# Performance work log

Hardware: AMD Instinct MI355X
Metric: run time of the kernel (lower is better)

Reference implementation:

```python
import jax, jax.numpy as jnp
import numpy as np

EPS = 1e-8

def setup_inputs() -> dict:
    key = jax.random.key(0)
    k1, k2, k3, k4, k5 = jax.random.split(key, 5)
    B, N, M, D = 64, 65536, 64, 256
    return {
        "embeddings": jax.random.normal(k1, (B, D), dtype=jnp.float32),
        "w_prev": jax.random.uniform(k2, (B, N), dtype=jnp.float32),
        "memory": jax.random.normal(k3, (B, N, M), dtype=jnp.float32),
        "W": jax.random.normal(k4, (D, M + 6), dtype=jnp.float32) * 0.05,
        "b": jax.random.normal(k5, (M + 6,), dtype=jnp.float32) * 0.01,
    }


def reference(embeddings, w_prev, memory, W, b):
    Mdim = memory.shape[-1]
    a = embeddings @ W + b  # [B, M+6]
    k = a[:, :Mdim]                                   # key
    beta = jax.nn.softplus(a[:, Mdim:Mdim + 1])       # key strength
    g = jax.nn.sigmoid(a[:, Mdim + 1:Mdim + 2])       # interpolation gate
    s = jax.nn.softmax(a[:, Mdim + 2:Mdim + 5], axis=1)  # 3-wide shift
    gamma = 1.0 + jax.nn.softplus(a[:, Mdim + 5:Mdim + 6])  # sharpening

    # content addressing: cosine similarity then softmax
    kn = k / (jnp.linalg.norm(k, axis=1, keepdims=True) + EPS)          # [B, M]
    mn = memory / (jnp.linalg.norm(memory, axis=2, keepdims=True) + EPS)  # [B, N, M]
    sim = jnp.einsum('bm,bnm->bn', kn, mn)                              # [B, N]
    wc = jax.nn.softmax(beta * sim, axis=1)

    # gated interpolation with previous weights
    wg = g * wc + (1.0 - g) * w_prev

    # circular shift convolution (shifts -1, 0, +1)
    wt = (s[:, 0:1] * jnp.roll(wg, 1, axis=1)
          + s[:, 1:2] * wg
          + s[:, 2:3] * jnp.roll(wg, -1, axis=1))

    # sharpening
    wp = wt ** gamma
    w = wp / (jnp.sum(wp, axis=1, keepdims=True) + EPS)

    # weighted memory read
    read = jnp.einsum('bn,bnm->bm', w, memory)
    return read, w
```

## Files before the change

### kernel.cpp

```cpp
#include <hip/hip_runtime.h>
#include <math.h>

#define EPS 1e-8f

constexpr int B = 64;
constexpr int N = 65536;
constexpr int M = 64;
constexpr int D = 256;
constexpr int A = M + 6;

constexpr size_t OFF_KN   = 0;
constexpr size_t OFF_SCAL = OFF_KN + (size_t)B * M;
constexpr size_t OFF_E    = OFF_SCAL + (size_t)B * 8;
constexpr size_t OFF_ZP   = OFF_E + (size_t)B * N;
constexpr size_t OFF_SP   = OFF_ZP + (size_t)B * 64;
constexpr size_t OFF_RP   = OFF_SP + (size_t)B * 16;

__device__ __forceinline__ float softplusf(float x) {
    return (x > 20.0f) ? x : log1pf(expf(x));
}

__global__ void k1_controller(const float* __restrict__ emb,
                              const float* __restrict__ Wm,
                              const float* __restrict__ bias,
                              float* __restrict__ kn,
                              float* __restrict__ scal) {
    int b = blockIdx.x;
    int t = threadIdx.x;
    __shared__ float se[D];
    __shared__ float sa[A];
    __shared__ float snorm;
    se[t] = emb[(size_t)b * D + t];
    __syncthreads();
    if (t < A) {
        float acc = bias[t];
        for (int d = 0; d < D; ++d) acc += se[d] * Wm[(size_t)d * A + t];
        sa[t] = acc;
    }
    __syncthreads();
    if (t == 0) {
        float s = 0.f;
        for (int j = 0; j < M; ++j) s += sa[j] * sa[j];
        snorm = sqrtf(s) + EPS;
        float beta = softplusf(sa[M]);
        float g = 1.f / (1.f + expf(-sa[M + 1]));
        float s0 = sa[M + 2], s1 = sa[M + 3], s2 = sa[M + 4];
        float mx = fmaxf(s0, fmaxf(s1, s2));
        float e0 = expf(s0 - mx), e1 = expf(s1 - mx), e2 = expf(s2 - mx);
        float Zs = e0 + e1 + e2;
        float gamma = 1.f + softplusf(sa[M + 5]);
        scal[b * 8 + 0] = beta;
        scal[b * 8 + 1] = g;
        scal[b * 8 + 2] = e0 / Zs;
        scal[b * 8 + 3] = e1 / Zs;
        scal[b * 8 + 4] = e2 / Zs;
        scal[b * 8 + 5] = gamma;
    }
    __syncthreads();
    if (t < M) kn[b * M + t] = sa[t] / snorm;
}

__global__ void k2_sim(const float* __restrict__ mem,
                       const float* __restrict__ kn,
                       const float* __restrict__ scal,
                       float* __restrict__ e,
                       float* __restrict__ zpart) {
    const int ROWS = 1024;
    int b = blockIdx.y;
    int base = blockIdx.x * ROWS;
    int t = threadIdx.x;
    int gid = t >> 4, q = t & 15;
    float beta = scal[b * 8 + 0];
    const float4 knq = reinterpret_cast<const float4*>(kn + (size_t)b * M)[q];
    const float4* mrow = reinterpret_cast<const float4*>(mem + (size_t)b * N * M);
    float* eb = e + (size_t)b * N;
    float lsum = 0.f;
    #pragma unroll 4
    for (int r = gid; r < ROWS; r += 16) {
        int n = base + r;
        float4 v = mrow[(size_t)n * 16 + q];
        float dot = v.x * knq.x + v.y * knq.y + v.z * knq.z + v.w * knq.w;
        float nrm = v.x * v.x + v.y * v.y + v.z * v.z + v.w * v.w;
        #pragma unroll
        for (int msk = 8; msk >= 1; msk >>= 1) {
            dot += __shfl_xor(dot, msk);
            nrm += __shfl_xor(nrm, msk);
        }
        float ev = expf(beta * (dot / (sqrtf(nrm) + EPS)));
        if (q == 0) { eb[n] = ev; lsum += ev; }
    }
    __shared__ float red[16];
    if (q == 0) red[gid] = lsum;
    __syncthreads();
    if (t == 0) {
        float s = 0.f;
        #pragma unroll
        for (int i = 0; i < 16; ++i) s += red[i];
        zpart[b * 64 + blockIdx.x] = s;
    }
}

__global__ void k4_wp(const float* __restrict__ e,
                      const float* __restrict__ wprev,
                      const float* __restrict__ scal,
                      const float* __restrict__ zpart,
                      float* __restrict__ wout,
                      float* __restrict__ spart) {
    int b = blockIdx.y;
    int bx = blockIdx.x;
    int t = threadIdx.x;
    float Z = 0.f;
    const float* zp = zpart + b * 64;
    #pragma unroll
    for (int i = 0; i < 64; ++i) Z += zp[i];
    float g   = scal[b * 8 + 1];
    float s0  = scal[b * 8 + 2];
    float s1  = scal[b * 8 + 3];
    float s2  = scal[b * 8 + 4];
    float gam = scal[b * 8 + 5];
    float c1 = g / Z;
    float c2 = 1.f - g;
    const float* eb = e + (size_t)b * N;
    const float* wb = wprev + (size_t)b * N;
    float* wo = wout + (size_t)b * N;
    float lsum = 0.f;
    #pragma unroll
    for (int i = 0; i < 4; ++i) {
        int n0 = bx * 4096 + (i * 256 + t) * 4;
        float4 e4 = *reinterpret_cast<const float4*>(eb + n0);
        float4 w4 = *reinterpret_cast<const float4*>(wb + n0);
        int nm = (n0 - 1) & (N - 1);
        int np = (n0 + 4) & (N - 1);
        float em = eb[nm], ep = eb[np];
        float wm = wb[nm], wp5 = wb[np];
        float wgm = c1 * em   + c2 * wm;
        float wg0 = c1 * e4.x + c2 * w4.x;
        float wg1 = c1 * e4.y + c2 * w4.y;
        float wg2 = c1 * e4.z + c2 * w4.z;
        float wg3 = c1 * e4.w + c2 * w4.w;
        float wg4 = c1 * ep   + c2 * wp5;
        float p0 = powf(s0 * wgm + s1 * wg0 + s2 * wg1, gam);
        float p1 = powf(s0 * wg0 + s1 * wg1 + s2 * wg2, gam);
        float p2 = powf(s0 * wg1 + s1 * wg2 + s2 * wg3, gam);
        float p3 = powf(s0 * wg2 + s1 * wg3 + s2 * wg4, gam);
        lsum += (p0 + p1) + (p2 + p3);
        *reinterpret_cast<float4*>(wo + n0) = make_float4(p0, p1, p2, p3);
    }
    __shared__ float red[256];
    red[t] = lsum;
    __syncthreads();
    for (int k = 128; k >= 1; k >>= 1) {
        if (t < k) red[t] += red[t + k];
        __syncthreads();
    }
    if (t == 0) spart[b * 16 + bx] = red[0];
}

__global__ void k5_read(const float* __restrict__ mem,
                        float* __restrict__ wout,
                        const float* __restrict__ spart,
                        float* __restrict__ readpart) {
    const int ROWS = 1024;
    int b = blockIdx.y;
    int base = blockIdx.x * ROWS;
    int t = threadIdx.x;
    int gid = t >> 4, q = t & 15;
    float S = 0.f;
    const float* sp = spart + b * 16;
    #pragma unroll
    for (int i = 0; i < 16; ++i) S += sp[i];
    float invS = 1.f / (S + EPS);
    const float4* mrow = reinterpret_cast<const float4*>(mem + (size_t)b * N * M);
    float* wb = wout + (size_t)b * N;
    float4 acc = make_float4(0.f, 0.f, 0.f, 0.f);
    #pragma unroll 4
    for (int r = gid; r < ROWS; r += 16) {
        int n = base + r;
        float wv = wb[n] * invS;
        float4 v = mrow[(size_t)n * 16 + q];
        acc.x += wv * v.x;
        acc.y += wv * v.y;
        acc.z += wv * v.z;
        acc.w += wv * v.w;
    }
    __shared__ float sacc[16][64];
    sacc[gid][q * 4 + 0] = acc.x;
    sacc[gid][q * 4 + 1] = acc.y;
    sacc[gid][q * 4 + 2] = acc.z;
    sacc[gid][q * 4 + 3] = acc.w;
    __syncthreads();
    #pragma unroll
    for (int i = 0; i < 4; ++i) {
        int n = base + i * 256 + t;
        wb[n] = wb[n] * invS;
    }
    if (t < 64) {
        float s = 0.f;
        #pragma unroll
        for (int g2 = 0; g2 < 16; ++g2) s += sacc[g2][t];
        readpart[((size_t)b * 64 + blockIdx.x) * 64 + t] = s;
    }
}

__global__ void k6_read_reduce(const float* __restrict__ readpart,
                               float* __restrict__ readout) {
    int b = blockIdx.x;
    int m = threadIdx.x;
    float s = 0.f;
    #pragma unroll
    for (int kb = 0; kb < 64; ++kb) s += readpart[((size_t)b * 64 + kb) * 64 + m];
    readout[b * 64 + m] = s;
}

extern "C" void kernel_launch(void* const* d_in, const int* in_sizes, int n_in,
                              void* d_out, int out_size, void* d_ws, size_t ws_size,
                              hipStream_t stream) {
    const float* emb   = (const float*)d_in[0];
    const float* wprev = (const float*)d_in[1];
    const float* mem   = (const float*)d_in[2];
    const float* Wm    = (const float*)d_in[3];
    const float* bias  = (const float*)d_in[4];

    float* out = (float*)d_out;
    float* readout = out;
    float* wout    = out + (size_t)B * M;

    float* ws = (float*)d_ws;
    float* kn   = ws + OFF_KN;
    float* scal = ws + OFF_SCAL;
    float* e    = ws + OFF_E;
    float* zp   = ws + OFF_ZP;
    float* sp   = ws + OFF_SP;
    float* rp   = ws + OFF_RP;

    k1_controller<<<dim3(B), dim3(256), 0, stream>>>(emb, Wm, bias, kn, scal);
    k2_sim<<<dim3(N / 1024, B), dim3(256), 0, stream>>>(mem, kn, scal, e, zp);
    k4_wp<<<dim3(N / 4096, B), dim3(256), 0, stream>>>(e, wprev, scal, zp, wout, sp);
    k5_read<<<dim3(N / 1024, B), dim3(256), 0, stream>>>(mem, wout, sp, rp);
    k6_read_reduce<<<dim3(B), dim3(64), 0, stream>>>(rp, readout);
}
```

Baseline: 457.7 us.

## Chunk batches and fuse shift/sharpen with read so memory rereads hit cache

Processes the batch in chunks of 8 so the similarity pass and the fused weighting+read pass touch a memory slice small enough to stay in the last-level cache. Fuses the interpolation, shift and sharpening into the read kernel, deferring normalization to a separate w-normalize kernel and scaling the reduced read by 1/S. Intent is to avoid a second full DRAM pass over the large memory tensor. Risks lower occupancy per chunk launch and redundant per-row scalar work in 16 lanes.

```diff
diff --git a/kernel.cpp b/kernel.cpp
--- a/kernel.cpp
+++ b/kernel.cpp
@@ -8,13 +8,14 @@
 constexpr int M = 64;
 constexpr int D = 256;
 constexpr int A = M + 6;
+constexpr int CHUNK = 8;
 
 constexpr size_t OFF_KN   = 0;
 constexpr size_t OFF_SCAL = OFF_KN + (size_t)B * M;
 constexpr size_t OFF_E    = OFF_SCAL + (size_t)B * 8;
 constexpr size_t OFF_ZP   = OFF_E + (size_t)B * N;
 constexpr size_t OFF_SP   = OFF_ZP + (size_t)B * 64;
-constexpr size_t OFF_RP   = OFF_SP + (size_t)B * 16;
+constexpr size_t OFF_RP   = OFF_SP + (size_t)B * 64;
 
 __device__ __forceinline__ float softplusf(float x) {
     return (x > 20.0f) ? x : log1pf(expf(x));
@@ -64,9 +65,10 @@
                        const float* __restrict__ kn,
                        const float* __restrict__ scal,
                        float* __restrict__ e,
-                       float* __restrict__ zpart) {
+                       float* __restrict__ zpart,
+                       int b0) {
     const int ROWS = 1024;
-    int b = blockIdx.y;
+    int b = b0 + blockIdx.y;
     int base = blockIdx.x * ROWS;
     int t = threadIdx.x;
     int gid = t >> 4, q = t & 15;
@@ -75,7 +77,7 @@
     const float4* mrow = reinterpret_cast<const float4*>(mem + (size_t)b * N * M);
     float* eb = e + (size_t)b * N;
     float lsum = 0.f;
-    #pragma unroll 4
+    #pragma unroll 8
     for (int r = gid; r < ROWS; r += 16) {
         int n = base + r;
         float4 v = mrow[(size_t)n * 16 + q];
@@ -100,15 +102,21 @@
     }
 }
 
-__global__ void k4_wp(const float* __restrict__ e,
-                      const float* __restrict__ wprev,
-                      const float* __restrict__ scal,
-                      const float* __restrict__ zpart,
-                      float* __restrict__ wout,
-                      float* __restrict__ spart) {
-    int b = blockIdx.y;
+__global__ void k45_fused(const float* __restrict__ mem,
+                          const float* __restrict__ e,
+                          const float* __restrict__ wprev,
+                          const float* __restrict__ scal,
+                          const float* __restrict__ zpart,
+                          float* __restrict__ wout,
+                          float* __restrict__ spart,
+                          float* __restrict__ readpart,
+                          int b0) {
+    const int ROWS = 1024;
+    int b = b0 + blockIdx.y;
     int bx = blockIdx.x;
+    int base = bx * ROWS;
     int t = threadIdx.x;
+    int gid = t >> 4, q = t & 15;
     float Z = 0.f;
     const float* zp = zpart + b * 64;
     #pragma unroll
@@ -120,96 +128,80 @@
     float gam = scal[b * 8 + 5];
     float c1 = g / Z;
     float c2 = 1.f - g;
+    const float4* mrow = reinterpret_cast<const float4*>(mem + (size_t)b * N * M);
     const float* eb = e + (size_t)b * N;
     const float* wb = wprev + (size_t)b * N;
     float* wo = wout + (size_t)b * N;
+    float4 acc = make_float4(0.f, 0.f, 0.f, 0.f);
     float lsum = 0.f;
-    #pragma unroll
-    for (int i = 0; i < 4; ++i) {
-        int n0 = bx * 4096 + (i * 256 + t) * 4;
-        float4 e4 = *reinterpret_cast<const float4*>(eb + n0);
-        float4 w4 = *reinterpret_cast<const float4*>(wb + n0);
-        int nm = (n0 - 1) & (N - 1);
-        int np = (n0 + 4) & (N - 1);
-        float em = eb[nm], ep = eb[np];
-        float wm = wb[nm], wp5 = wb[np];
-        float wgm = c1 * em   + c2 * wm;
-        float wg0 = c1 * e4.x + c2 * w4.x;
-        float wg1 = c1 * e4.y + c2 * w4.y;
-        float wg2 = c1 * e4.z + c2 * w4.z;
-        float wg3 = c1 * e4.w + c2 * w4.w;
-        float wg4 = c1 * ep   + c2 * wp5;
-        float p0 = powf(s0 * wgm + s1 * wg0 + s2 * wg1, gam);
-        float p1 = powf(s0 * wg0 + s1 * wg1 + s2 * wg2, gam);
-        float p2 = powf(s0 * wg1 + s1 * wg2 + s2 * wg3, gam);
-        float p3 = powf(s0 * wg2 + s1 * wg3 + s2 * wg4, gam);
-        lsum += (p0 + p1) + (p2 + p3);
-        *reinterpret_cast<float4*>(wo + n0) = make_float4(p0, p1, p2, p3);
-    }
-    __shared__ float red[256];
-    red[t] = lsum;
-    __syncthreads();
-    for (int k = 128; k >= 1; k >>= 1) {
-        if (t < k) red[t] += red[t + k];
-        __syncthreads();
-    }
-    if (t == 0) spart[b * 16 + bx] = red[0];
-}
-
-__global__ void k5_read(const float* __restrict__ mem,
-                        float* __restrict__ wout,
-                        const float* __restrict__ spart,
-                        float* __restrict__ readpart) {
-    const int ROWS = 1024;
-    int b = blockIdx.y;
-    int base = blockIdx.x * ROWS;
-    int t = threadIdx.x;
-    int gid = t >> 4, q = t & 15;
-    float S = 0.f;
-    const float* sp = spart + b * 16;
-    #pragma unroll
-    for (int i = 0; i < 16; ++i) S += sp[i];
-    float invS = 1.f / (S + EPS);
-    const float4* mrow = reinterpret_cast<const float4*>(mem + (size_t)b * N * M);
-    float* wb = wout + (size_t)b * N;
-    float4 acc = make_float4(0.f, 0.f, 0.f, 0.f);
     #pragma unroll 4
     for (int r = gid; r < ROWS; r += 16) {
         int n = base + r;
-        float wv = wb[n] * invS;
+        int nm = (n - 1) & (N - 1);
+        int np = (n + 1) & (N - 1);
+        float wgm = c1 * eb[nm] + c2 * wb[nm];
+        float wg0 = c1 * eb[n]  + c2 * wb[n];
+        float wgp = c1 * eb[np] + c2 * wb[np];
+        float wt = s0 * wgm + s1 * wg0 + s2 * wgp;
+        float wp = powf(wt, gam);
         float4 v = mrow[(size_t)n * 16 + q];
-        acc.x += wv * v.x;
-        acc.y += wv * v.y;
-        acc.z += wv * v.z;
-        acc.w += wv * v.w;
+        acc.x += wp * v.x;
+        acc.y += wp * v.y;
+        acc.z += wp * v.z;
+        acc.w += wp * v.w;
+        if (q == 0) { wo[n] = wp; lsum += wp; }
     }
     __shared__ float sacc[16][64];
+    __shared__ float sred[16];
     sacc[gid][q * 4 + 0] = acc.x;
     sacc[gid][q * 4 + 1] = acc.y;
     sacc[gid][q * 4 + 2] = acc.z;
     sacc[gid][q * 4 + 3] = acc.w;
-    __syncthreads();
-    #pragma unroll
-    for (int i = 0; i < 4; ++i) {
-        int n = base + i * 256 + t;
-        wb[n] = wb[n] * invS;
-    }
+    if (q == 0) sred[gid] = lsum;
+    __syncthreads();
     if (t < 64) {
         float s = 0.f;
         #pragma unroll
         for (int g2 = 0; g2 < 16; ++g2) s += sacc[g2][t];
-        readpart[((size_t)b * 64 + blockIdx.x) * 64 + t] = s;
-    }
+        readpart[((size_t)b * 64 + bx) * 64 + t] = s;
+    }
+    if (t == 0) {
+        float s = 0.f;
+        #pragma unroll
+        for (int i = 0; i < 16; ++i) s += sred[i];
+        spart[b * 64 + bx] = s;
+    }
+}
+
+__global__ void k7_wnorm(float* __restrict__ wout,
+                         const float* __restrict__ spart) {
+    int b = blockIdx.y;
+    float S = 0.f;
+    const float* sp = spart + b * 64;
+    #pragma unroll
+    for (int i = 0; i < 64; ++i) S += sp[i];
+    float invS = 1.f / (S + EPS);
+    size_t idx = (size_t)b * (N / 4) + blockIdx.x * 256 + threadIdx.x;
+    float4* w4 = reinterpret_cast<float4*>(wout);
+    float4 v = w4[idx];
+    v.x *= invS; v.y *= invS; v.z *= invS; v.w *= invS;
+    w4[idx] = v;
 }
 
 __global__ void k6_read_reduce(const float* __restrict__ readpart,
+                               const float* __restrict__ spart,
                                float* __restrict__ readout) {
     int b = blockIdx.x;
     int m = threadIdx.x;
+    float S = 0.f;
+    const float* sp = spart + b * 64;
+    #pragma unroll
+    for (int i = 0; i < 64; ++i) S += sp[i];
+    float invS = 1.f / (S + EPS);
     float s = 0.f;
     #pragma unroll
     for (int kb = 0; kb < 64; ++kb) s += readpart[((size_t)b * 64 + kb) * 64 + m];
-    readout[b * 64 + m] = s;
+    readout[b * 64 + m] = s * invS;
 }
 
 extern "C" void kernel_launch(void* const* d_in, const int* in_sizes, int n_in,
@@ -234,8 +226,12 @@
     float* rp   = ws + OFF_RP;
 
     k1_controller<<<dim3(B), dim3(256), 0, stream>>>(emb, Wm, bias, kn, scal);
-    k2_sim<<<dim3(N / 1024, B), dim3(256), 0, stream>>>(mem, kn, scal, e, zp);
-    k4_wp<<<dim3(N / 4096, B), dim3(256), 0, stream>>>(e, wprev, scal, zp, wout, sp);
-    k5_read<<<dim3(N / 1024, B), dim3(256), 0, stream>>>(mem, wout, sp, rp);
-    k6_read_reduce<<<dim3(B), dim3(64), 0, stream>>>(rp, readout);
-}
+    for (int c = 0; c < B / CHUNK; ++c) {
+        int b0 = c * CHUNK;
+        k2_sim<<<dim3(64, CHUNK), dim3(256), 0, stream>>>(mem, kn, scal, e, zp, b0);
+        k45_fused<<<dim3(64, CHUNK), dim3(256), 0, stream>>>(mem, e, wprev, scal, zp,
+                                                             wout, sp, rp, b0);
+    }
+    k7_wnorm<<<dim3(64, B), dim3(256), 0, stream>>>(wout, sp);
+    k6_read_reduce<<<dim3(B), dim3(64), 0, stream>>>(rp, sp, readout);
+}
```

Result: slower. 1.043 ms (+127.9%).

## Fuse sharpening with weighted read and defer normalization to an epilogue

Applied to the files above, without the earlier changes.

The sharpening/weight computation and the weighted memory read are merged into one kernel that keeps the unnormalized sharpened weights in shared memory, so the read no longer reloads w from global. Normalization by the global sum is deferred: the read partials are scaled by 1/S in a combined epilogue that also rescales w and reduces the read partials, replacing two separate kernels. Memory loads also switch to nontemporal loads with a larger unroll. This trades one fewer launch and less w traffic for a separate rescale pass over w.

```diff
diff --git a/kernel.cpp b/kernel.cpp
--- a/kernel.cpp
+++ b/kernel.cpp
@@ -9,12 +9,14 @@
 constexpr int D = 256;
 constexpr int A = M + 6;
 
+typedef float vfloat4 __attribute__((ext_vector_type(4)));
+
 constexpr size_t OFF_KN   = 0;
 constexpr size_t OFF_SCAL = OFF_KN + (size_t)B * M;
 constexpr size_t OFF_E    = OFF_SCAL + (size_t)B * 8;
 constexpr size_t OFF_ZP   = OFF_E + (size_t)B * N;
 constexpr size_t OFF_SP   = OFF_ZP + (size_t)B * 64;
-constexpr size_t OFF_RP   = OFF_SP + (size_t)B * 16;
+constexpr size_t OFF_RP   = OFF_SP + (size_t)B * 64;
 
 __device__ __forceinline__ float softplusf(float x) {
     return (x > 20.0f) ? x : log1pf(expf(x));
@@ -71,14 +73,14 @@
     int t = threadIdx.x;
     int gid = t >> 4, q = t & 15;
     float beta = scal[b * 8 + 0];
-    const float4 knq = reinterpret_cast<const float4*>(kn + (size_t)b * M)[q];
-    const float4* mrow = reinterpret_cast<const float4*>(mem + (size_t)b * N * M);
+    const vfloat4 knq = reinterpret_cast<const vfloat4*>(kn + (size_t)b * M)[q];
+    const vfloat4* mrow = reinterpret_cast<const vfloat4*>(mem + (size_t)b * N * M);
     float* eb = e + (size_t)b * N;
     float lsum = 0.f;
-    #pragma unroll 4
+    #pragma unroll 8
     for (int r = gid; r < ROWS; r += 16) {
         int n = base + r;
-        float4 v = mrow[(size_t)n * 16 + q];
+        vfloat4 v = __builtin_nontemporal_load(&mrow[(size_t)n * 16 + q]);
         float dot = v.x * knq.x + v.y * knq.y + v.z * knq.z + v.w * knq.w;
         float nrm = v.x * v.x + v.y * v.y + v.z * v.z + v.w * v.w;
         #pragma unroll
@@ -100,15 +102,25 @@
     }
 }
 
-__global__ void k4_wp(const float* __restrict__ e,
-                      const float* __restrict__ wprev,
-                      const float* __restrict__ scal,
-                      const float* __restrict__ zpart,
-                      float* __restrict__ wout,
-                      float* __restrict__ spart) {
+__global__ void k45_fused(const float* __restrict__ mem,
+                          const float* __restrict__ e,
+                          const float* __restrict__ wprev,
+                          const float* __restrict__ scal,
+                          const float* __restrict__ zpart,
+                          float* __restrict__ wout,
+                          float* __restrict__ spart,
+                          float* __restrict__ readpart) {
+    const int ROWS = 1024;
     int b = blockIdx.y;
     int bx = blockIdx.x;
-    int t = threadIdx.x;
+    int base = bx * ROWS;
+    int t = threadIdx.x;
+    int gid = t >> 4, q = t & 15;
+
+    __shared__ float s_wp[ROWS];
+    __shared__ float red[256];
+    __shared__ float sacc[16][64];
+
     float Z = 0.f;
     const float* zp = zpart + b * 64;
     #pragma unroll
@@ -120,96 +132,92 @@
     float gam = scal[b * 8 + 5];
     float c1 = g / Z;
     float c2 = 1.f - g;
+
     const float* eb = e + (size_t)b * N;
     const float* wb = wprev + (size_t)b * N;
     float* wo = wout + (size_t)b * N;
-    float lsum = 0.f;
-    #pragma unroll
-    for (int i = 0; i < 4; ++i) {
-        int n0 = bx * 4096 + (i * 256 + t) * 4;
-        float4 e4 = *reinterpret_cast<const float4*>(eb + n0);
-        float4 w4 = *reinterpret_cast<const float4*>(wb + n0);
+
+    {
+        int n0 = base + t * 4;
+        vfloat4 e4 = *reinterpret_cast<const vfloat4*>(eb + n0);
+        vfloat4 w4 = *reinterpret_cast<const vfloat4*>(wb + n0);
         int nm = (n0 - 1) & (N - 1);
         int np = (n0 + 4) & (N - 1);
         float em = eb[nm], ep = eb[np];
-        float wm = wb[nm], wp5 = wb[np];
+        float wm = wb[nm], wpp = wb[np];
         float wgm = c1 * em   + c2 * wm;
         float wg0 = c1 * e4.x + c2 * w4.x;
         float wg1 = c1 * e4.y + c2 * w4.y;
         float wg2 = c1 * e4.z + c2 * w4.z;
         float wg3 = c1 * e4.w + c2 * w4.w;
-        float wg4 = c1 * ep   + c2 * wp5;
+        float wg4 = c1 * ep   + c2 * wpp;
         float p0 = powf(s0 * wgm + s1 * wg0 + s2 * wg1, gam);
         float p1 = powf(s0 * wg0 + s1 * wg1 + s2 * wg2, gam);
         float p2 = powf(s0 * wg1 + s1 * wg2 + s2 * wg3, gam);
         float p3 = powf(s0 * wg2 + s1 * wg3 + s2 * wg4, gam);
-        lsum += (p0 + p1) + (p2 + p3);
-        *reinterpret_cast<float4*>(wo + n0) = make_float4(p0, p1, p2, p3);
-    }
-    __shared__ float red[256];
-    red[t] = lsum;
-    __syncthreads();
-    for (int k = 128; k >= 1; k >>= 1) {
-        if (t < k) red[t] += red[t + k];
-        __syncthreads();
-    }
-    if (t == 0) spart[b * 16 + bx] = red[0];
-}
-
-__global__ void k5_read(const float* __restrict__ mem,
-                        float* __restrict__ wout,
-                        const float* __restrict__ spart,
-                        float* __restrict__ readpart) {
-    const int ROWS = 1024;
-    int b = blockIdx.y;
-    int base = blockIdx.x * ROWS;
-    int t = threadIdx.x;
-    int gid = t >> 4, q = t & 15;
-    float S = 0.f;
-    const float* sp = spart + b * 16;
-    #pragma unroll
-    for (int i = 0; i < 16; ++i) S += sp[i];
-    float invS = 1.f / (S + EPS);
-    const float4* mrow = reinterpret_cast<const float4*>(mem + (size_t)b * N * M);
-    float* wb = wout + (size_t)b * N;
-    float4 acc = make_float4(0.f, 0.f, 0.f, 0.f);
-    #pragma unroll 4
+        s_wp[t * 4 + 0] = p0;
+        s_wp[t * 4 + 1] = p1;
+        s_wp[t * 4 + 2] = p2;
+        s_wp[t * 4 + 3] = p3;
+        vfloat4 pv; pv.x = p0; pv.y = p1; pv.z = p2; pv.w = p3;
+        *reinterpret_cast<vfloat4*>(wo + n0) = pv;
+        red[t] = (p0 + p1) + (p2 + p3);
+    }
+    __syncthreads();
+
+    const vfloat4* mrow = reinterpret_cast<const vfloat4*>(mem + (size_t)b * N * M);
+    vfloat4 acc = (vfloat4)0.f;
+    #pragma unroll 8
     for (int r = gid; r < ROWS; r += 16) {
-        int n = base + r;
-        float wv = wb[n] * invS;
-        float4 v = mrow[(size_t)n * 16 + q];
-        acc.x += wv * v.x;
-        acc.y += wv * v.y;
-        acc.z += wv * v.z;
-        acc.w += wv * v.w;
-    }
-    __shared__ float sacc[16][64];
+        float wp = s_wp[r];
+        vfloat4 v = __builtin_nontemporal_load(&mrow[(size_t)(base + r) * 16 + q]);
+        acc.x += wp * v.x;
+        acc.y += wp * v.y;
+        acc.z += wp * v.z;
+        acc.w += wp * v.w;
+    }
     sacc[gid][q * 4 + 0] = acc.x;
     sacc[gid][q * 4 + 1] = acc.y;
     sacc[gid][q * 4 + 2] = acc.z;
     sacc[gid][q * 4 + 3] = acc.w;
     __syncthreads();
+    if (t < 64) {
+        float s = 0.f;
+        #pragma unroll
+        for (int g2 = 0; g2 < 16; ++g2) s += sacc[g2][t];
+        readpart[((size_t)b * 64 + bx) * 64 + t] = s;
+    }
+    for (int k = 128; k >= 1; k >>= 1) {
+        if (t < k) red[t] += red[t + k];
+        __syncthreads();
+    }
+    if (t == 0) spart[b * 64 + bx] = red[0];
+}
+
+__global__ void k67_epilogue(float* __restrict__ wout,
+                             const float* __restrict__ spart,
+                             const float* __restrict__ readpart,
+                             float* __restrict__ readout) {
+    int b = blockIdx.y;
+    int bx = blockIdx.x;
+    int t = threadIdx.x;
+    float S = 0.f;
+    const float* sp = spart + b * 64;
     #pragma unroll
-    for (int i = 0; i < 4; ++i) {
-        int n = base + i * 256 + t;
-        wb[n] = wb[n] * invS;
-    }
-    if (t < 64) {
-        float s = 0.f;
-        #pragma unroll
-        for (int g2 = 0; g2 < 16; ++g2) s += sacc[g2][t];
-        readpart[((size_t)b * 64 + blockIdx.x) * 64 + t] = s;
-    }
-}
-
-__global__ void k6_read_reduce(const float* __restrict__ readpart,
-                               float* __restrict__ readout) {
-    int b = blockIdx.x;
-    int m = threadIdx.x;
-    float s = 0.f;
-    #pragma unroll
-    for (int kb = 0; kb < 64; ++kb) s += readpart[((size_t)b * 64 + kb) * 64 + m];
-    readout[b * 64 + m] = s;
+    for (int i = 0; i < 64; ++i) S += sp[i];
+    float invS = 1.f / (S + EPS);
+    if (bx < 64) {
+        size_t idx = (size_t)b * (N / 4) + (size_t)bx * 256 + t;
+        vfloat4* w4 = reinterpret_cast<vfloat4*>(wout);
+        vfloat4 v = w4[idx];
+        v.x *= invS; v.y *= invS; v.z *= invS; v.w *= invS;
+        w4[idx] = v;
+    } else if (t < 64) {
+        float s = 0.f;
+        #pragma unroll
+        for (int kb = 0; kb < 64; ++kb) s += readpart[((size_t)b * 64 + kb) * 64 + t];
+        readout[b * 64 + t] = s * invS;
+    }
 }
 
 extern "C" void kernel_launch(void* const* d_in, const int* in_sizes, int n_in,
@@ -234,8 +242,8 @@
     float* rp   = ws + OFF_RP;
 
     k1_controller<<<dim3(B), dim3(256), 0, stream>>>(emb, Wm, bias, kn, scal);
-    k2_sim<<<dim3(N / 1024, B), dim3(256), 0, stream>>>(mem, kn, scal, e, zp);
-    k4_wp<<<dim3(N / 4096, B), dim3(256), 0, stream>>>(e, wprev, scal, zp, wout, sp);
-    k5_read<<<dim3(N / 1024, B), dim3(256), 0, stream>>>(mem, wout, sp, rp);
-    k6_read_reduce<<<dim3(B), dim3(64), 0, stream>>>(rp, readout);
-}
+    k2_sim<<<dim3(64, B), dim3(256), 0, stream>>>(mem, kn, scal, e, zp);
+    k45_fused<<<dim3(64, B), dim3(256), 0, stream>>>(mem, e, wprev, scal, zp,
+                                                     wout, sp, rp);
+    k67_epilogue<<<dim3(65, B), dim3(256), 0, stream>>>(wout, sp, rp, readout);
+}
```

Result: faster. 390.1 us, median of 2 (-14.8%).
